# Kernel tuning notes

Measured on AMD Instinct MI355X. Metric: run time of the kernel, lower is better.

The kernel has to match this reference:

```python
import jax, jax.numpy as jnp
import numpy as np

HEADS = 16
D_MODEL = 1024
D_H = D_MODEL // HEADS


def setup_inputs() -> dict:
    key = jax.random.key(0)
    ks = jax.random.split(key, 11)
    B, S = 4, 2048
    scale = 1.0 / np.sqrt(D_MODEL)
    inp = {
        "q": jax.random.normal(ks[0], (B, S, D_MODEL), dtype=jnp.float32),
        "k": jax.random.normal(ks[1], (B, S, D_MODEL), dtype=jnp.float32),
        "v": jax.random.normal(ks[2], (B, S, D_MODEL), dtype=jnp.float32),
        "Wq": jax.random.normal(ks[3], (D_MODEL, D_MODEL), dtype=jnp.float32) * scale,
        "bq": jnp.zeros((D_MODEL,), dtype=jnp.float32),
        "Wk": jax.random.normal(ks[4], (D_MODEL, D_MODEL), dtype=jnp.float32) * scale,
        "bk": jnp.zeros((D_MODEL,), dtype=jnp.float32),
        "Wv": jax.random.normal(ks[5], (D_MODEL, D_MODEL), dtype=jnp.float32) * scale,
        "bv": jnp.zeros((D_MODEL,), dtype=jnp.float32),
        "Wo": jax.random.normal(ks[6], (D_MODEL, D_MODEL), dtype=jnp.float32) * scale,
        "bo": jnp.zeros((D_MODEL,), dtype=jnp.float32),
    }
    return inp


def reference(q, k, v, Wq, bq, Wk, bk, Wv, bv, Wo, bo):
    B, S, _ = q.shape
    # torch Linear: x @ W.T + b
    qh = (q @ Wq.T + bq).reshape(B, S, HEADS, D_H).transpose(0, 2, 1, 3)  # b h s d
    kh = (k @ Wk.T + bk).reshape(B, S, HEADS, D_H).transpose(0, 2, 1, 3)
    vh = (v @ Wv.T + bv).reshape(B, S, HEADS, D_H).transpose(0, 2, 1, 3)
    logits = jnp.einsum("bhsd,bhtd->bhst", qh, kh) / jnp.sqrt(jnp.float32(D_H))
    attn = jax.nn.softmax(logits, axis=-1)
    ctx = jnp.einsum("bhst,bhtd->bhsd", attn, vh)
    concat = ctx.transpose(0, 2, 1, 3).reshape(B, S, D_MODEL)
    return concat @ Wo.T + bo
```

## Files before the change

kernel.cpp:

```cpp
#include <hip/hip_runtime.h>
#include <hip/hip_bf16.h>
#include <stdint.h>

#define B_SZ 4
#define S_SZ 2048
#define DM   1024
#define NH   16
#define DH   64

typedef short short8 __attribute__((ext_vector_type(8)));
typedef float f32x4 __attribute__((ext_vector_type(4)));

typedef const __attribute__((address_space(1))) uint32_t* gp_t;
typedef __attribute__((address_space(3))) uint32_t* lp_t;

__device__ __forceinline__ void gload16(const void* g, void* l) {
  __builtin_amdgcn_global_load_lds((gp_t)g, (lp_t)l, 16, 0, 0);
}

__device__ __forceinline__ unsigned short f2b(float f) {
  __hip_bfloat16 h = __float2bfloat16(f);
  return *reinterpret_cast<unsigned short*>(&h);
}

__global__ void cast_acts(const float* __restrict__ a, const float* __restrict__ b,
                          const float* __restrict__ c,
                          unsigned short* __restrict__ oa, unsigned short* __restrict__ ob,
                          unsigned short* __restrict__ oc) {
  int i = blockIdx.x * blockDim.x + threadIdx.x;
  int which = i >> 21;
  int j = i & ((1 << 21) - 1);
  const float* src = which == 0 ? a : (which == 1 ? b : c);
  unsigned short* dst = which == 0 ? oa : (which == 1 ? ob : oc);
  float4 v = reinterpret_cast<const float4*>(src)[j];
  ushort4 o;
  o.x = f2b(v.x); o.y = f2b(v.y); o.z = f2b(v.z); o.w = f2b(v.w);
  reinterpret_cast<ushort4*>(dst)[j] = o;
}

__global__ void cast_w4(const float* __restrict__ a, const float* __restrict__ b,
                        const float* __restrict__ c, const float* __restrict__ d,
                        unsigned short* __restrict__ oa, unsigned short* __restrict__ ob,
                        unsigned short* __restrict__ oc, unsigned short* __restrict__ od) {
  int i = blockIdx.x * blockDim.x + threadIdx.x;
  int which = i >> 18;
  int j = i & ((1 << 18) - 1);
  const float* src = which == 0 ? a : (which == 1 ? b : (which == 2 ? c : d));
  unsigned short* dst = which == 0 ? oa : (which == 1 ? ob : (which == 2 ? oc : od));
  float4 v = reinterpret_cast<const float4*>(src)[j];
  ushort4 o;
  o.x = f2b(v.x); o.y = f2b(v.y); o.z = f2b(v.z); o.w = f2b(v.w);
  reinterpret_cast<ushort4*>(dst)[j] = o;
}

__global__ __launch_bounds__(256)
void gemm_qkv(const unsigned short* __restrict__ Aq, const unsigned short* __restrict__ Ak,
              const unsigned short* __restrict__ Av,
              const unsigned short* __restrict__ Wq, const unsigned short* __restrict__ Wk,
              const unsigned short* __restrict__ Wv,
              const float* __restrict__ bq, const float* __restrict__ bk,
              const float* __restrict__ bv,
              unsigned short* __restrict__ Qh, unsigned short* __restrict__ Kh,
              unsigned short* __restrict__ Vth, float qscale)
{
  constexpr int K = DM;
  __shared__ unsigned short lA[128 * 64];
  __shared__ unsigned short lB[128 * 64];
  const int tid  = threadIdx.x;
  const int lane = tid & 63;
  const int wave = tid >> 6;

  const int cpx = gridDim.x >> 3;
  const int bid = blockIdx.x;
  const int wg  = (bid & 7) * cpx + (bid >> 3);
  const int which = wg >> 9;
  const int rest  = wg & 511;
  const int bm = rest >> 3;
  const int bn = rest & 7;

  const unsigned short* A  = which == 0 ? Aq : (which == 1 ? Ak : Av);
  const unsigned short* Bw = which == 0 ? Wq : (which == 1 ? Wk : Wv);
  const float* bias        = which == 0 ? bq : (which == 1 ? bk : bv);
  const float scale        = which == 0 ? qscale : 1.0f;

  const int wm = (wave >> 1) << 6;
  const int wn = (wave & 1) << 6;

  f32x4 acc[4][4] = {};

  const int r0 = tid >> 3;
  const int sl = tid & 7;
  const unsigned short* Abase = A + (size_t)(bm * 128) * K;
  const unsigned short* Bbase = Bw + (size_t)(bn * 128) * K;

  for (int k0 = 0; k0 < K; k0 += 64) {
#pragma unroll
    for (int i = 0; i < 4; ++i) {
      int row = i * 32 + r0;
      int gs  = sl ^ (row & 7);
      gload16(Abase + (size_t)row * K + k0 + gs * 8, lA + (i * 256 + wave * 64) * 8);
      gload16(Bbase + (size_t)row * K + k0 + gs * 8, lB + (i * 256 + wave * 64) * 8);
    }
    __syncthreads();
#pragma unroll
    for (int ks = 0; ks < 2; ++ks) {
      short8 af[4], bf[4];
#pragma unroll
      for (int f = 0; f < 4; ++f) {
        int rowa = wm + f * 16 + (lane & 15);
        int sa   = ((ks * 4) + (lane >> 4)) ^ (rowa & 7);
        af[f] = *reinterpret_cast<const short8*>(&lA[rowa * 64 + sa * 8]);
        int rowb = wn + f * 16 + (lane & 15);
        int sb   = ((ks * 4) + (lane >> 4)) ^ (rowb & 7);
        bf[f] = *reinterpret_cast<const short8*>(&lB[rowb * 64 + sb * 8]);
      }
#pragma unroll
      for (int i = 0; i < 4; ++i)
#pragma unroll
        for (int j = 0; j < 4; ++j)
          acc[i][j] = __builtin_amdgcn_mfma_f32_16x16x32_bf16(af[i], bf[j], acc[i][j], 0, 0, 0);
    }
    __syncthreads();
  }

  float bv4[4];
#pragma unroll
  for (int j = 0; j < 4; ++j)
    bv4[j] = bias[bn * 128 + wn + j * 16 + (lane & 15)];

#pragma unroll
  for (int i = 0; i < 4; ++i) {
    int m0 = bm * 128 + wm + i * 16 + ((lane >> 4) << 2);
#pragma unroll
    for (int j = 0; j < 4; ++j) {
      int n = bn * 128 + wn + j * 16 + (lane & 15);
      if (which < 2) {
        unsigned short* o = which == 0 ? Qh : Kh;
#pragma unroll
        for (int r = 0; r < 4; ++r) {
          int m = m0 + r;
          size_t idx = ((size_t)((m >> 11) * NH + (n >> 6)) * S_SZ + (m & 2047)) * DH + (n & 63);
          o[idx] = f2b((acc[i][j][r] + bv4[j]) * scale);
        }
      } else {
        size_t idx = ((size_t)((m0 >> 11) * NH + (n >> 6)) * DH + (n & 63)) * S_SZ + (m0 & 2047);
        ushort4 pk;
        pk.x = f2b(acc[i][j][0] + bv4[j]);
        pk.y = f2b(acc[i][j][1] + bv4[j]);
        pk.z = f2b(acc[i][j][2] + bv4[j]);
        pk.w = f2b(acc[i][j][3] + bv4[j]);
        *reinterpret_cast<ushort4*>(&Vth[idx]) = pk;
      }
    }
  }
}

template<int MODE>
__global__ __launch_bounds__(256)
void gemm_bt(const unsigned short* __restrict__ A,
             const unsigned short* __restrict__ Bw,
             const float* __restrict__ bias,
             void* __restrict__ out,
             int M, int N, int K, float scale)
{
  __shared__ unsigned short lA[128 * 64];
  __shared__ unsigned short lB[128 * 64];
  const int tid  = threadIdx.x;
  const int lane = tid & 63;
  const int wave = tid >> 6;

  const int cpx = gridDim.x >> 3;
  const int bid = blockIdx.x;
  const int wg  = (bid & 7) * cpx + (bid >> 3);
  const int nbn = N >> 7;
  const int bm  = wg / nbn;
  const int bn  = wg % nbn;

  const int wm = (wave >> 1) << 6;
  const int wn = (wave & 1) << 6;

  f32x4 acc[4][4] = {};

  const int r0 = tid >> 3;
  const int sl = tid & 7;
  const unsigned short* Abase = A + (size_t)(bm * 128) * K;
  const unsigned short* Bbase = Bw + (size_t)(bn * 128) * K;

  for (int k0 = 0; k0 < K; k0 += 64) {
#pragma unroll
    for (int i = 0; i < 4; ++i) {
      int row = i * 32 + r0;
      int gs  = sl ^ (row & 7);
      gload16(Abase + (size_t)row * K + k0 + gs * 8, lA + (i * 256 + wave * 64) * 8);
      gload16(Bbase + (size_t)row * K + k0 + gs * 8, lB + (i * 256 + wave * 64) * 8);
    }
    __syncthreads();
#pragma unroll
    for (int ks = 0; ks < 2; ++ks) {
      short8 af[4], bf[4];
#pragma unroll
      for (int f = 0; f < 4; ++f) {
        int rowa = wm + f * 16 + (lane & 15);
        int sa   = ((ks * 4) + (lane >> 4)) ^ (rowa & 7);
        af[f] = *reinterpret_cast<const short8*>(&lA[rowa * 64 + sa * 8]);
        int rowb = wn + f * 16 + (lane & 15);
        int sb   = ((ks * 4) + (lane >> 4)) ^ (rowb & 7);
        bf[f] = *reinterpret_cast<const short8*>(&lB[rowb * 64 + sb * 8]);
      }
#pragma unroll
      for (int i = 0; i < 4; ++i)
#pragma unroll
        for (int j = 0; j < 4; ++j)
          acc[i][j] = __builtin_amdgcn_mfma_f32_16x16x32_bf16(af[i], bf[j], acc[i][j], 0, 0, 0);
    }
    __syncthreads();
  }

  float bv[4];
#pragma unroll
  for (int j = 0; j < 4; ++j)
    bv[j] = bias[bn * 128 + wn + j * 16 + (lane & 15)];

#pragma unroll
  for (int i = 0; i < 4; ++i) {
    int m0 = bm * 128 + wm + i * 16 + ((lane >> 4) << 2);
#pragma unroll
    for (int j = 0; j < 4; ++j) {
      int n = bn * 128 + wn + j * 16 + (lane & 15);
      float* o = (float*)out;
#pragma unroll
      for (int r = 0; r < 4; ++r)
        o[(size_t)(m0 + r) * N + n] = acc[i][j][r] + bv[j];
    }
  }
}

__global__ __launch_bounds__(256, 4)
void attn_kernel(const unsigned short* __restrict__ Q,
                 const unsigned short* __restrict__ Kc,
                 const unsigned short* __restrict__ Vt,
                 unsigned short* __restrict__ ctx)
{
  __shared__ unsigned short lK[2][64 * 64];
  __shared__ unsigned short lV[64 * 64];
  __shared__ unsigned short lP[4][16 * 64];

  const int tid  = threadIdx.x;
  const int lane = tid & 63;
  const int wave = tid >> 6;
  const int hi   = lane >> 4;
  const int lo   = lane & 15;

  const int bid = blockIdx.x;
  const int xcd = bid & 7;
  const int idx = bid >> 3;
  const int stile = idx & 15;
  const int bh    = ((idx >> 4) << 3) + xcd;
  const int b = bh >> 4, h = bh & 15;

  const int s0 = stile * 128 + wave * 32;

  short8 qf[2][2];
#pragma unroll
  for (int fm = 0; fm < 2; ++fm)
#pragma unroll
    for (int ks = 0; ks < 2; ++ks) {
      int s = s0 + fm * 16 + lo;
      int c = ks * 32 + hi * 8;
      qf[fm][ks] = *reinterpret_cast<const short8*>(&Q[((size_t)bh * S_SZ + s) * DH + c]);
    }

  f32x4 cacc[2][4] = {};
  f32x4 lacc[2] = {};

  short8 onesb;
#pragma unroll
  for (int i = 0; i < 8; ++i) onesb[i] = (short)0x3F80;

  const int r0 = tid >> 3;
  const int sl = tid & 7;
  const unsigned short* Kbh = Kc + (size_t)bh * S_SZ * DH;
  const unsigned short* Vbh = Vt + (size_t)bh * DH * S_SZ;

#define STAGE_K(bb, t0)                                                            \
  _Pragma("unroll")                                                                \
  for (int i = 0; i < 2; ++i) {                                                    \
    int row = i * 32 + r0;                                                         \
    int gs  = sl ^ (row & 7);                                                      \
    gload16(Kbh + ((size_t)(t0) + row) * DH + gs * 8, lK[bb] + (i * 256 + wave * 64) * 8); \
  }
#define STAGE_V(t0)                                                                \
  _Pragma("unroll")                                                                \
  for (int i = 0; i < 2; ++i) {                                                    \
    int row = i * 32 + r0;                                                         \
    int gs  = sl ^ (row & 7);                                                      \
    gload16(Vbh + (size_t)row * S_SZ + (t0) + gs * 8, lV + (i * 256 + wave * 64) * 8); \
  }

  STAGE_K(0, 0)

  unsigned short* Pw = &lP[wave][0];
  const int NT = S_SZ / 64;

  for (int it = 0; it < NT; ++it) {
    const int cb = it & 1;
    __syncthreads();
    STAGE_V(it * 64)
    { int nk = (it + 1 < NT) ? (it + 1) * 64 : 0;
      STAGE_K(cb ^ 1, nk) }

    f32x4 lg[4][2];
#pragma unroll
    for (int fn = 0; fn < 4; ++fn)
#pragma unroll
      for (int fm = 0; fm < 2; ++fm)
        lg[fn][fm] = f32x4{-8.f, -8.f, -8.f, -8.f};
    __builtin_amdgcn_s_setprio(1);
#pragma unroll
    for (int ks = 0; ks < 2; ++ks) {
      short8 kf[4];
#pragma unroll
      for (int fn = 0; fn < 4; ++fn) {
        int row = fn * 16 + lo;
        int s2  = ((ks * 4) + hi) ^ (row & 7);
        kf[fn] = *reinterpret_cast<const short8*>(&lK[cb][row * 64 + s2 * 8]);
      }
#pragma unroll
      for (int fn = 0; fn < 4; ++fn)
#pragma unroll
        for (int fm = 0; fm < 2; ++fm)
          lg[fn][fm] = __builtin_amdgcn_mfma_f32_16x16x32_bf16(kf[fn], qf[fm][ks], lg[fn][fm], 0, 0, 0);
    }
    __builtin_amdgcn_s_setprio(0);

    short8 pa[2][2];
    const int psw = (lo & 7) ^ (((lo >> 3) & 1) << 2);
#pragma unroll
    for (int fm = 0; fm < 2; ++fm) {
#pragma unroll
      for (int fn = 0; fn < 4; ++fn) {
        int pslot = (fn * 2 + (hi >> 1)) ^ psw;
        int paddr = lo * 64 + pslot * 8 + (hi & 1) * 4;
        ushort4 pk;
        pk.x = f2b(exp2f(lg[fn][fm][0]));
        pk.y = f2b(exp2f(lg[fn][fm][1]));
        pk.z = f2b(exp2f(lg[fn][fm][2]));
        pk.w = f2b(exp2f(lg[fn][fm][3]));
        *reinterpret_cast<ushort4*>(&Pw[paddr]) = pk;
      }
#pragma unroll
      for (int ks = 0; ks < 2; ++ks) {
        int s2 = ((ks * 4) + hi) ^ psw;
        pa[fm][ks] = *reinterpret_cast<const short8*>(&Pw[lo * 64 + s2 * 8]);
      }
    }

    asm volatile("s_waitcnt vmcnt(2)" ::: "memory");
    __builtin_amdgcn_s_barrier();
    __builtin_amdgcn_sched_barrier(0);

    __builtin_amdgcn_s_setprio(1);
#pragma unroll
    for (int ks = 0; ks < 2; ++ks) {
      short8 vbf[4];
#pragma unroll
      for (int fn = 0; fn < 4; ++fn) {
        int row = fn * 16 + lo;
        int s2  = ((ks * 4) + hi) ^ (row & 7);
        vbf[fn] = *reinterpret_cast<const short8*>(&lV[row * 64 + s2 * 8]);
      }
#pragma unroll
      for (int fm = 0; fm < 2; ++fm) {
#pragma unroll
        for (int fn = 0; fn < 4; ++fn)
          cacc[fm][fn] = __builtin_amdgcn_mfma_f32_16x16x32_bf16(pa[fm][ks], vbf[fn], cacc[fm][fn], 0, 0, 0);
        lacc[fm] = __builtin_amdgcn_mfma_f32_16x16x32_bf16(pa[fm][ks], onesb, lacc[fm], 0, 0, 0);
      }
    }
    __builtin_amdgcn_s_setprio(0);
  }

#pragma unroll
  for (int fm = 0; fm < 2; ++fm)
#pragma unroll
    for (int r = 0; r < 4; ++r) {
      float inv = 1.0f / lacc[fm][r];
      int s = s0 + fm * 16 + hi * 4 + r;
#pragma unroll
      for (int fn = 0; fn < 4; ++fn) {
        int d = fn * 16 + lo;
        ctx[(((size_t)b * S_SZ + s) * NH + h) * DH + d] = f2b(cacc[fm][fn][r] * inv);
      }
    }
}

extern "C" void kernel_launch(void* const* d_in, const int* in_sizes, int n_in,
                              void* d_out, int out_size, void* d_ws, size_t ws_size,
                              hipStream_t stream)
{
  const float* q  = (const float*)d_in[0];
  const float* k  = (const float*)d_in[1];
  const float* v  = (const float*)d_in[2];
  const float* Wq = (const float*)d_in[3];
  const float* bq = (const float*)d_in[4];
  const float* Wk = (const float*)d_in[5];
  const float* bk = (const float*)d_in[6];
  const float* Wv = (const float*)d_in[7];
  const float* bv = (const float*)d_in[8];
  const float* Wo = (const float*)d_in[9];
  const float* bo = (const float*)d_in[10];

  constexpr size_t N_ACT = (size_t)B_SZ * S_SZ * DM;
  constexpr size_t N_W   = (size_t)DM * DM;
  constexpr size_t SZ_ACT = N_ACT * 2;
  constexpr size_t SZ_W   = N_W * 2;

  char* ws = (char*)d_ws;
  unsigned short* qb  = (unsigned short*)(ws);
  unsigned short* kb  = (unsigned short*)(ws + SZ_ACT);
  unsigned short* vb_ = (unsigned short*)(ws + 2 * SZ_ACT);
  unsigned short* Wqb = (unsigned short*)(ws + 3 * SZ_ACT);
  unsigned short* Wkb = (unsigned short*)(ws + 3 * SZ_ACT + SZ_W);
  unsigned short* Wvb = (unsigned short*)(ws + 3 * SZ_ACT + 2 * SZ_W);
  unsigned short* Wob = (unsigned short*)(ws + 3 * SZ_ACT + 3 * SZ_W);
  unsigned short* Qh  = (unsigned short*)(ws + 3 * SZ_ACT + 4 * SZ_W);
  unsigned short* Kh  = (unsigned short*)(ws + 4 * SZ_ACT + 4 * SZ_W);
  unsigned short* Vth = (unsigned short*)(ws + 5 * SZ_ACT + 4 * SZ_W);
  unsigned short* ctx = qb;

  cast_acts<<<(int)(3 * (N_ACT / 4) / 256), 256, 0, stream>>>(q, k, v, qb, kb, vb_);
  cast_w4<<<(int)(4 * (N_W / 4) / 256), 256, 0, stream>>>(Wq, Wk, Wv, Wo, Wqb, Wkb, Wvb, Wob);

  const float qscale = 0.18033688011112042f;

  gemm_qkv<<<1536, 256, 0, stream>>>(qb, kb, vb_, Wqb, Wkb, Wvb, bq, bk, bv,
                                     Qh, Kh, Vth, qscale);

  attn_kernel<<<B_SZ * NH * (S_SZ / 128), 256, 0, stream>>>(Qh, Kh, Vth, ctx);

  gemm_bt<2><<<512, 256, 0, stream>>>(ctx, Wob, bo, d_out, 8192, DM, DM, 1.0f);
}
```

Baseline: 223.7 us.

## Halve attention query tile and stage K through registers into single LDS buffer

The attention kernel now processes 64 query rows per block (16 per wave) instead of 128, which doubles the grid size. K tiles are now prefetched into registers with ordinary global loads and written into one LDS buffer after the PV step, replacing the double-buffered global_load_lds path. This frees LDS and registers and adds parallelism, but it doubles K/V global traffic per query and halves the MFMA work done per staged tile.

```diff
diff --git a/kernel.cpp b/kernel.cpp
--- a/kernel.cpp
+++ b/kernel.cpp
@@ -10,6 +10,7 @@
 
 typedef short short8 __attribute__((ext_vector_type(8)));
 typedef float f32x4 __attribute__((ext_vector_type(4)));
+typedef uint32_t uint32x4 __attribute__((ext_vector_type(4)));
 
 typedef const __attribute__((address_space(1))) uint32_t* gp_t;
 typedef __attribute__((address_space(3))) uint32_t* lp_t;
@@ -241,7 +242,7 @@
                  const unsigned short* __restrict__ Vt,
                  unsigned short* __restrict__ ctx)
 {
-  __shared__ unsigned short lK[2][64 * 64];
+  __shared__ unsigned short lK[64 * 64];
   __shared__ unsigned short lV[64 * 64];
   __shared__ unsigned short lP[4][16 * 64];
 
@@ -254,24 +255,22 @@
   const int bid = blockIdx.x;
   const int xcd = bid & 7;
   const int idx = bid >> 3;
-  const int stile = idx & 15;
-  const int bh    = ((idx >> 4) << 3) + xcd;
+  const int stile = idx & 31;
+  const int bh    = ((idx >> 5) << 3) + xcd;
   const int b = bh >> 4, h = bh & 15;
 
-  const int s0 = stile * 128 + wave * 32;
-
-  short8 qf[2][2];
-#pragma unroll
-  for (int fm = 0; fm < 2; ++fm)
-#pragma unroll
-    for (int ks = 0; ks < 2; ++ks) {
-      int s = s0 + fm * 16 + lo;
-      int c = ks * 32 + hi * 8;
-      qf[fm][ks] = *reinterpret_cast<const short8*>(&Q[((size_t)bh * S_SZ + s) * DH + c]);
-    }
-
-  f32x4 cacc[2][4] = {};
-  f32x4 lacc[2] = {};
+  const int s0 = stile * 64 + wave * 16;
+
+  short8 qf[2];
+#pragma unroll
+  for (int ks = 0; ks < 2; ++ks) {
+    int s = s0 + lo;
+    int c = ks * 32 + hi * 8;
+    qf[ks] = *reinterpret_cast<const short8*>(&Q[((size_t)bh * S_SZ + s) * DH + c]);
+  }
+
+  f32x4 cacc[4] = {};
+  f32x4 lacc = {};
 
   short8 onesb;
 #pragma unroll
@@ -282,13 +281,19 @@
   const unsigned short* Kbh = Kc + (size_t)bh * S_SZ * DH;
   const unsigned short* Vbh = Vt + (size_t)bh * DH * S_SZ;
 
-#define STAGE_K(bb, t0)                                                            \
+  uint32x4 kr[2];
+
+#define LOADK(t0)                                                                  \
   _Pragma("unroll")                                                                \
   for (int i = 0; i < 2; ++i) {                                                    \
     int row = i * 32 + r0;                                                         \
     int gs  = sl ^ (row & 7);                                                      \
-    gload16(Kbh + ((size_t)(t0) + row) * DH + gs * 8, lK[bb] + (i * 256 + wave * 64) * 8); \
-  }
+    kr[i] = *reinterpret_cast<const uint32x4*>(&Kbh[((size_t)(t0) + row) * DH + gs * 8]); \
+  }
+#define WRITEK()                                                                   \
+  _Pragma("unroll")                                                                \
+  for (int i = 0; i < 2; ++i)                                                      \
+    *reinterpret_cast<uint32x4*>(&lK[i * 2048 + wave * 512 + lane * 8]) = kr[i];
 #define STAGE_V(t0)                                                                \
   _Pragma("unroll")                                                                \
   for (int i = 0; i < 2; ++i) {                                                    \
@@ -297,24 +302,24 @@
     gload16(Vbh + (size_t)row * S_SZ + (t0) + gs * 8, lV + (i * 256 + wave * 64) * 8); \
   }
 
-  STAGE_K(0, 0)
+  LOADK(0)
+  asm volatile("s_waitcnt vmcnt(0)" ::: "memory");
+  WRITEK()
 
   unsigned short* Pw = &lP[wave][0];
   const int NT = S_SZ / 64;
 
   for (int it = 0; it < NT; ++it) {
-    const int cb = it & 1;
     __syncthreads();
     STAGE_V(it * 64)
+    __builtin_amdgcn_sched_barrier(0);
     { int nk = (it + 1 < NT) ? (it + 1) * 64 : 0;
-      STAGE_K(cb ^ 1, nk) }
-
-    f32x4 lg[4][2];
+      LOADK(nk) }
+
+    f32x4 lg[4];
 #pragma unroll
     for (int fn = 0; fn < 4; ++fn)
-#pragma unroll
-      for (int fm = 0; fm < 2; ++fm)
-        lg[fn][fm] = f32x4{-8.f, -8.f, -8.f, -8.f};
+      lg[fn] = f32x4{-8.f, -8.f, -8.f, -8.f};
     __builtin_amdgcn_s_setprio(1);
 #pragma unroll
     for (int ks = 0; ks < 2; ++ks) {
@@ -323,36 +328,31 @@
       for (int fn = 0; fn < 4; ++fn) {
         int row = fn * 16 + lo;
         int s2  = ((ks * 4) + hi) ^ (row & 7);
-        kf[fn] = *reinterpret_cast<const short8*>(&lK[cb][row * 64 + s2 * 8]);
+        kf[fn] = *reinterpret_cast<const short8*>(&lK[row * 64 + s2 * 8]);
       }
 #pragma unroll
       for (int fn = 0; fn < 4; ++fn)
-#pragma unroll
-        for (int fm = 0; fm < 2; ++fm)
-          lg[fn][fm] = __builtin_amdgcn_mfma_f32_16x16x32_bf16(kf[fn], qf[fm][ks], lg[fn][fm], 0, 0, 0);
+        lg[fn] = __builtin_amdgcn_mfma_f32_16x16x32_bf16(kf[fn], qf[ks], lg[fn], 0, 0, 0);
     }
     __builtin_amdgcn_s_setprio(0);
 
-    short8 pa[2][2];
+    short8 pa[2];
     const int psw = (lo & 7) ^ (((lo >> 3) & 1) << 2);
 #pragma unroll
-    for (int fm = 0; fm < 2; ++fm) {
-#pragma unroll
-      for (int fn = 0; fn < 4; ++fn) {
-        int pslot = (fn * 2 + (hi >> 1)) ^ psw;
-        int paddr = lo * 64 + pslot * 8 + (hi & 1) * 4;
-        ushort4 pk;
-        pk.x = f2b(exp2f(lg[fn][fm][0]));
-        pk.y = f2b(exp2f(lg[fn][fm][1]));
-        pk.z = f2b(exp2f(lg[fn][fm][2]));
-        pk.w = f2b(exp2f(lg[fn][fm][3]));
-        *reinterpret_cast<ushort4*>(&Pw[paddr]) = pk;
-      }
-#pragma unroll
-      for (int ks = 0; ks < 2; ++ks) {
-        int s2 = ((ks * 4) + hi) ^ psw;
-        pa[fm][ks] = *reinterpret_cast<const short8*>(&Pw[lo * 64 + s2 * 8]);
-      }
+    for (int fn = 0; fn < 4; ++fn) {
+      int pslot = (fn * 2 + (hi >> 1)) ^ psw;
+      int paddr = lo * 64 + pslot * 8 + (hi & 1) * 4;
+      ushort4 pk;
+      pk.x = f2b(exp2f(lg[fn][0]));
+      pk.y = f2b(exp2f(lg[fn][1]));
+      pk.z = f2b(exp2f(lg[fn][2]));
+      pk.w = f2b(exp2f(lg[fn][3]));
+      *reinterpret_cast<ushort4*>(&Pw[paddr]) = pk;
+    }
+#pragma unroll
+    for (int ks = 0; ks < 2; ++ks) {
+      int s2 = ((ks * 4) + hi) ^ psw;
+      pa[ks] = *reinterpret_cast<const short8*>(&Pw[lo * 64 + s2 * 8]);
     }
 
     asm volatile("s_waitcnt vmcnt(2)" ::: "memory");
@@ -370,28 +370,26 @@
         vbf[fn] = *reinterpret_cast<const short8*>(&lV[row * 64 + s2 * 8]);
       }
 #pragma unroll
-      for (int fm = 0; fm < 2; ++fm) {
-#pragma unroll
-        for (int fn = 0; fn < 4; ++fn)
-          cacc[fm][fn] = __builtin_amdgcn_mfma_f32_16x16x32_bf16(pa[fm][ks], vbf[fn], cacc[fm][fn], 0, 0, 0);
-        lacc[fm] = __builtin_amdgcn_mfma_f32_16x16x32_bf16(pa[fm][ks], onesb, lacc[fm], 0, 0, 0);
-      }
+      for (int fn = 0; fn < 4; ++fn)
+        cacc[fn] = __builtin_amdgcn_mfma_f32_16x16x32_bf16(pa[ks], vbf[fn], cacc[fn], 0, 0, 0);
+      lacc = __builtin_amdgcn_mfma_f32_16x16x32_bf16(pa[ks], onesb, lacc, 0, 0, 0);
     }
     __builtin_amdgcn_s_setprio(0);
-  }
-
-#pragma unroll
-  for (int fm = 0; fm < 2; ++fm)
-#pragma unroll
-    for (int r = 0; r < 4; ++r) {
-      float inv = 1.0f / lacc[fm][r];
-      int s = s0 + fm * 16 + hi * 4 + r;
-#pragma unroll
-      for (int fn = 0; fn < 4; ++fn) {
-        int d = fn * 16 + lo;
-        ctx[(((size_t)b * S_SZ + s) * NH + h) * DH + d] = f2b(cacc[fm][fn][r] * inv);
-      }
-    }
+
+    asm volatile("s_waitcnt vmcnt(0)" ::: "memory");
+    WRITEK()
+  }
+
+#pragma unroll
+  for (int r = 0; r < 4; ++r) {
+    float inv = 1.0f / lacc[r];
+    int s = s0 + hi * 4 + r;
+#pragma unroll
+    for (int fn = 0; fn < 4; ++fn) {
+      int d = fn * 16 + lo;
+      ctx[(((size_t)b * S_SZ + s) * NH + h) * DH + d] = f2b(cacc[fn][r] * inv);
+    }
+  }
 }
 
 extern "C" void kernel_launch(void* const* d_in, const int* in_sizes, int n_in,
@@ -436,7 +434,7 @@
   gemm_qkv<<<1536, 256, 0, stream>>>(qb, kb, vb_, Wqb, Wkb, Wvb, bq, bk, bv,
                                      Qh, Kh, Vth, qscale);
 
-  attn_kernel<<<B_SZ * NH * (S_SZ / 128), 256, 0, stream>>>(Qh, Kh, Vth, ctx);
+  attn_kernel<<<B_SZ * NH * (S_SZ / 64), 256, 0, stream>>>(Qh, Kh, Vth, ctx);
 
   gemm_bt<2><<<512, 256, 0, stream>>>(ctx, Wob, bo, d_out, 8192, DM, DM, 1.0f);
 }
```

Measured after the change: 230.6 us. 3.1% more time.

## Double KV tile to 128 and prefetch K through registers

Applied to the files above, without the earlier changes.

The attention loop now handles 128 keys per iteration instead of 64, halving the number of iterations and barriers. K tiles are prefetched into registers with plain global loads and written to a single LDS buffer after the PV stage, replacing the double-buffered global-to-LDS loads. V staging uses a wider 128-column layout with a new swizzle. This raises register pressure and LDS footprint, which may reduce occupancy under the launch bounds of 4 blocks per CU.

```diff
diff --git a/kernel.cpp b/kernel.cpp
--- a/kernel.cpp
+++ b/kernel.cpp
@@ -10,6 +10,7 @@
 
 typedef short short8 __attribute__((ext_vector_type(8)));
 typedef float f32x4 __attribute__((ext_vector_type(4)));
+typedef uint32_t uint32x4 __attribute__((ext_vector_type(4)));
 
 typedef const __attribute__((address_space(1))) uint32_t* gp_t;
 typedef __attribute__((address_space(3))) uint32_t* lp_t;
@@ -241,8 +242,8 @@
                  const unsigned short* __restrict__ Vt,
                  unsigned short* __restrict__ ctx)
 {
-  __shared__ unsigned short lK[2][64 * 64];
-  __shared__ unsigned short lV[64 * 64];
+  __shared__ unsigned short lK[128 * 64];
+  __shared__ unsigned short lV[64 * 128];
   __shared__ unsigned short lP[4][16 * 64];
 
   const int tid  = threadIdx.x;
@@ -282,92 +283,103 @@
   const unsigned short* Kbh = Kc + (size_t)bh * S_SZ * DH;
   const unsigned short* Vbh = Vt + (size_t)bh * DH * S_SZ;
 
-#define STAGE_K(bb, t0)                                                            \
+  uint32x4 kr[4];
+
+#define LOADK(t0)                                                                  \
   _Pragma("unroll")                                                                \
-  for (int i = 0; i < 2; ++i) {                                                    \
+  for (int i = 0; i < 4; ++i) {                                                    \
     int row = i * 32 + r0;                                                         \
     int gs  = sl ^ (row & 7);                                                      \
-    gload16(Kbh + ((size_t)(t0) + row) * DH + gs * 8, lK[bb] + (i * 256 + wave * 64) * 8); \
-  }
+    kr[i] = *reinterpret_cast<const uint32x4*>(&Kbh[((size_t)(t0) + row) * DH + gs * 8]); \
+  }
+#define WRITEK()                                                                   \
+  _Pragma("unroll")                                                                \
+  for (int i = 0; i < 4; ++i)                                                      \
+    *reinterpret_cast<uint32x4*>(&lK[i * 2048 + wave * 512 + lane * 8]) = kr[i];
 #define STAGE_V(t0)                                                                \
   _Pragma("unroll")                                                                \
-  for (int i = 0; i < 2; ++i) {                                                    \
-    int row = i * 32 + r0;                                                         \
-    int gs  = sl ^ (row & 7);                                                      \
-    gload16(Vbh + (size_t)row * S_SZ + (t0) + gs * 8, lV + (i * 256 + wave * 64) * 8); \
-  }
-
-  STAGE_K(0, 0)
+  for (int i = 0; i < 4; ++i) {                                                    \
+    int rowv = i * 16 + wave * 4 + hi;                                             \
+    int gsv  = lo ^ (wave * 4 + hi);                                               \
+    gload16(Vbh + (size_t)rowv * S_SZ + (t0) + gsv * 8, lV + (i * 256 + wave * 64) * 8); \
+  }
+
+  LOADK(0)
+  asm volatile("s_waitcnt vmcnt(0)" ::: "memory");
+  WRITEK()
 
   unsigned short* Pw = &lP[wave][0];
-  const int NT = S_SZ / 64;
+  const int NT = S_SZ / 128;
 
   for (int it = 0; it < NT; ++it) {
-    const int cb = it & 1;
     __syncthreads();
-    STAGE_V(it * 64)
-    { int nk = (it + 1 < NT) ? (it + 1) * 64 : 0;
-      STAGE_K(cb ^ 1, nk) }
-
-    f32x4 lg[4][2];
-#pragma unroll
-    for (int fn = 0; fn < 4; ++fn)
-#pragma unroll
-      for (int fm = 0; fm < 2; ++fm)
-        lg[fn][fm] = f32x4{-8.f, -8.f, -8.f, -8.f};
-    __builtin_amdgcn_s_setprio(1);
-#pragma unroll
-    for (int ks = 0; ks < 2; ++ks) {
-      short8 kf[4];
-#pragma unroll
-      for (int fn = 0; fn < 4; ++fn) {
-        int row = fn * 16 + lo;
-        int s2  = ((ks * 4) + hi) ^ (row & 7);
-        kf[fn] = *reinterpret_cast<const short8*>(&lK[cb][row * 64 + s2 * 8]);
-      }
-#pragma unroll
-      for (int fn = 0; fn < 4; ++fn)
+    STAGE_V(it * 128)
+    __builtin_amdgcn_sched_barrier(0);
+    { int nk = (it + 1 < NT) ? (it + 1) * 128 : 0;
+      LOADK(nk) }
+
+    short8 pa[2][4];
+    const int psw = (lo & 7) ^ (((lo >> 3) & 1) << 2);
+#pragma unroll
+    for (int hh = 0; hh < 2; ++hh) {
+      f32x4 lg[4][2];
+#pragma unroll
+      for (int f = 0; f < 4; ++f)
 #pragma unroll
         for (int fm = 0; fm < 2; ++fm)
-          lg[fn][fm] = __builtin_amdgcn_mfma_f32_16x16x32_bf16(kf[fn], qf[fm][ks], lg[fn][fm], 0, 0, 0);
-    }
-    __builtin_amdgcn_s_setprio(0);
-
-    short8 pa[2][2];
-    const int psw = (lo & 7) ^ (((lo >> 3) & 1) << 2);
-#pragma unroll
-    for (int fm = 0; fm < 2; ++fm) {
-#pragma unroll
-      for (int fn = 0; fn < 4; ++fn) {
-        int pslot = (fn * 2 + (hi >> 1)) ^ psw;
-        int paddr = lo * 64 + pslot * 8 + (hi & 1) * 4;
-        ushort4 pk;
-        pk.x = f2b(exp2f(lg[fn][fm][0]));
-        pk.y = f2b(exp2f(lg[fn][fm][1]));
-        pk.z = f2b(exp2f(lg[fn][fm][2]));
-        pk.w = f2b(exp2f(lg[fn][fm][3]));
-        *reinterpret_cast<ushort4*>(&Pw[paddr]) = pk;
-      }
+          lg[f][fm] = f32x4{-8.f, -8.f, -8.f, -8.f};
+      __builtin_amdgcn_s_setprio(1);
 #pragma unroll
       for (int ks = 0; ks < 2; ++ks) {
-        int s2 = ((ks * 4) + hi) ^ psw;
-        pa[fm][ks] = *reinterpret_cast<const short8*>(&Pw[lo * 64 + s2 * 8]);
-      }
-    }
-
-    asm volatile("s_waitcnt vmcnt(2)" ::: "memory");
+        short8 kf[4];
+#pragma unroll
+        for (int f = 0; f < 4; ++f) {
+          int rowk = (hh * 4 + f) * 16 + lo;
+          int s2   = ((ks * 4) + hi) ^ (rowk & 7);
+          kf[f] = *reinterpret_cast<const short8*>(&lK[rowk * 64 + s2 * 8]);
+        }
+#pragma unroll
+        for (int f = 0; f < 4; ++f)
+#pragma unroll
+          for (int fm = 0; fm < 2; ++fm)
+            lg[f][fm] = __builtin_amdgcn_mfma_f32_16x16x32_bf16(kf[f], qf[fm][ks], lg[f][fm], 0, 0, 0);
+      }
+      __builtin_amdgcn_s_setprio(0);
+
+#pragma unroll
+      for (int fm = 0; fm < 2; ++fm) {
+#pragma unroll
+        for (int f = 0; f < 4; ++f) {
+          int pslot = (f * 2 + (hi >> 1)) ^ psw;
+          int paddr = lo * 64 + pslot * 8 + (hi & 1) * 4;
+          ushort4 pk;
+          pk.x = f2b(exp2f(lg[f][fm][0]));
+          pk.y = f2b(exp2f(lg[f][fm][1]));
+          pk.z = f2b(exp2f(lg[f][fm][2]));
+          pk.w = f2b(exp2f(lg[f][fm][3]));
+          *reinterpret_cast<ushort4*>(&Pw[paddr]) = pk;
+        }
+#pragma unroll
+        for (int kh = 0; kh < 2; ++kh) {
+          int s2 = ((kh * 4) + hi) ^ psw;
+          pa[fm][hh * 2 + kh] = *reinterpret_cast<const short8*>(&Pw[lo * 64 + s2 * 8]);
+        }
+      }
+    }
+
+    asm volatile("s_waitcnt vmcnt(4)" ::: "memory");
     __builtin_amdgcn_s_barrier();
     __builtin_amdgcn_sched_barrier(0);
 
     __builtin_amdgcn_s_setprio(1);
 #pragma unroll
-    for (int ks = 0; ks < 2; ++ks) {
+    for (int ks = 0; ks < 4; ++ks) {
       short8 vbf[4];
 #pragma unroll
       for (int fn = 0; fn < 4; ++fn) {
-        int row = fn * 16 + lo;
-        int s2  = ((ks * 4) + hi) ^ (row & 7);
-        vbf[fn] = *reinterpret_cast<const short8*>(&lV[row * 64 + s2 * 8]);
+        int rowv = fn * 16 + lo;
+        int s2   = ((ks * 4) + hi) ^ lo;
+        vbf[fn] = *reinterpret_cast<const short8*>(&lV[rowv * 128 + s2 * 8]);
       }
 #pragma unroll
       for (int fm = 0; fm < 2; ++fm) {
@@ -378,6 +390,9 @@
       }
     }
     __builtin_amdgcn_s_setprio(0);
+
+    asm volatile("s_waitcnt vmcnt(0)" ::: "memory");
+    WRITEK()
   }
 
 #pragma unroll
```

Measured after the change: 388.6 us. 1.74x slower.

## Split attention over key halves and merge partial contexts in a separate kernel

Applied to the files above, without the earlier changes.

Each attention block now handles only half of the key sequence, which doubles the grid and writes unnormalized bf16 context plus row sums per half. A new merge kernel adds the two partial contexts and divides by the summed denominators. K staging changes from async global-to-LDS double buffering to a register prefetch written to a single LDS buffer after the PV step, which frees LDS. This buys more parallelism and occupancy at the cost of an extra kernel pass over the context and extra bf16 rounding of the partial sums. The merge is valid without max tracking because the softmax logits use a fixed offset.

```diff
diff --git a/kernel.cpp b/kernel.cpp
--- a/kernel.cpp
+++ b/kernel.cpp
@@ -10,6 +10,7 @@
 
 typedef short short8 __attribute__((ext_vector_type(8)));
 typedef float f32x4 __attribute__((ext_vector_type(4)));
+typedef uint32_t uint32x4 __attribute__((ext_vector_type(4)));
 
 typedef const __attribute__((address_space(1))) uint32_t* gp_t;
 typedef __attribute__((address_space(3))) uint32_t* lp_t;
@@ -21,6 +22,10 @@
 __device__ __forceinline__ unsigned short f2b(float f) {
   __hip_bfloat16 h = __float2bfloat16(f);
   return *reinterpret_cast<unsigned short*>(&h);
+}
+__device__ __forceinline__ float b2f(unsigned short u) {
+  uint32_t w = (uint32_t)u << 16;
+  return __builtin_bit_cast(float, w);
 }
 
 __global__ void cast_acts(const float* __restrict__ a, const float* __restrict__ b,
@@ -239,9 +244,12 @@
 void attn_kernel(const unsigned short* __restrict__ Q,
                  const unsigned short* __restrict__ Kc,
                  const unsigned short* __restrict__ Vt,
-                 unsigned short* __restrict__ ctx)
+                 unsigned short* __restrict__ c0,
+                 unsigned short* __restrict__ c1,
+                 float* __restrict__ l0,
+                 float* __restrict__ l1)
 {
-  __shared__ unsigned short lK[2][64 * 64];
+  __shared__ unsigned short lK[64 * 64];
   __shared__ unsigned short lV[64 * 64];
   __shared__ unsigned short lP[4][16 * 64];
 
@@ -254,11 +262,13 @@
   const int bid = blockIdx.x;
   const int xcd = bid & 7;
   const int idx = bid >> 3;
-  const int stile = idx & 15;
-  const int bh    = ((idx >> 4) << 3) + xcd;
+  const int half  = idx & 1;
+  const int stile = (idx >> 1) & 15;
+  const int bh    = ((idx >> 5) << 3) + xcd;
   const int b = bh >> 4, h = bh & 15;
 
   const int s0 = stile * 128 + wave * 32;
+  const int tbase = half * (S_SZ / 2);
 
   short8 qf[2][2];
 #pragma unroll
@@ -282,13 +292,19 @@
   const unsigned short* Kbh = Kc + (size_t)bh * S_SZ * DH;
   const unsigned short* Vbh = Vt + (size_t)bh * DH * S_SZ;
 
-#define STAGE_K(bb, t0)                                                            \
+  uint32x4 kr[2];
+
+#define LOADK(t0)                                                                  \
   _Pragma("unroll")                                                                \
   for (int i = 0; i < 2; ++i) {                                                    \
     int row = i * 32 + r0;                                                         \
     int gs  = sl ^ (row & 7);                                                      \
-    gload16(Kbh + ((size_t)(t0) + row) * DH + gs * 8, lK[bb] + (i * 256 + wave * 64) * 8); \
-  }
+    kr[i] = *reinterpret_cast<const uint32x4*>(&Kbh[((size_t)(t0) + row) * DH + gs * 8]); \
+  }
+#define WRITEK()                                                                   \
+  _Pragma("unroll")                                                                \
+  for (int i = 0; i < 2; ++i)                                                      \
+    *reinterpret_cast<uint32x4*>(&lK[i * 2048 + wave * 512 + lane * 8]) = kr[i];
 #define STAGE_V(t0)                                                                \
   _Pragma("unroll")                                                                \
   for (int i = 0; i < 2; ++i) {                                                    \
@@ -297,17 +313,19 @@
     gload16(Vbh + (size_t)row * S_SZ + (t0) + gs * 8, lV + (i * 256 + wave * 64) * 8); \
   }
 
-  STAGE_K(0, 0)
+  LOADK(tbase)
+  asm volatile("s_waitcnt vmcnt(0)" ::: "memory");
+  WRITEK()
 
   unsigned short* Pw = &lP[wave][0];
-  const int NT = S_SZ / 64;
+  const int NT = (S_SZ / 2) / 64;
 
   for (int it = 0; it < NT; ++it) {
-    const int cb = it & 1;
     __syncthreads();
-    STAGE_V(it * 64)
-    { int nk = (it + 1 < NT) ? (it + 1) * 64 : 0;
-      STAGE_K(cb ^ 1, nk) }
+    STAGE_V(tbase + it * 64)
+    __builtin_amdgcn_sched_barrier(0);
+    { int nk = (it + 1 < NT) ? tbase + (it + 1) * 64 : tbase;
+      LOADK(nk) }
 
     f32x4 lg[4][2];
 #pragma unroll
@@ -323,7 +341,7 @@
       for (int fn = 0; fn < 4; ++fn) {
         int row = fn * 16 + lo;
         int s2  = ((ks * 4) + hi) ^ (row & 7);
-        kf[fn] = *reinterpret_cast<const short8*>(&lK[cb][row * 64 + s2 * 8]);
+        kf[fn] = *reinterpret_cast<const short8*>(&lK[row * 64 + s2 * 8]);
       }
 #pragma unroll
       for (int fn = 0; fn < 4; ++fn)
@@ -378,20 +396,51 @@
       }
     }
     __builtin_amdgcn_s_setprio(0);
-  }
-
+
+    asm volatile("s_waitcnt vmcnt(0)" ::: "memory");
+    WRITEK()
+  }
+
+  unsigned short* cdst = half ? c1 : c0;
+  float* ldst = half ? l1 : l0;
 #pragma unroll
   for (int fm = 0; fm < 2; ++fm)
 #pragma unroll
     for (int r = 0; r < 4; ++r) {
-      float inv = 1.0f / lacc[fm][r];
       int s = s0 + fm * 16 + hi * 4 + r;
 #pragma unroll
       for (int fn = 0; fn < 4; ++fn) {
         int d = fn * 16 + lo;
-        ctx[(((size_t)b * S_SZ + s) * NH + h) * DH + d] = f2b(cacc[fm][fn][r] * inv);
-      }
-    }
+        cdst[(((size_t)b * S_SZ + s) * NH + h) * DH + d] = f2b(cacc[fm][fn][r]);
+      }
+      if (lo == 0) ldst[(size_t)bh * S_SZ + s] = lacc[fm][r];
+    }
+}
+
+__global__ void merge_ctx(const unsigned short* __restrict__ c0,
+                          const unsigned short* __restrict__ c1,
+                          const float* __restrict__ l0,
+                          const float* __restrict__ l1,
+                          unsigned short* __restrict__ ctx)
+{
+  int i = blockIdx.x * blockDim.x + threadIdx.x;
+  int rh = i >> 3;
+  int h  = rh & 15;
+  int bs = rh >> 4;
+  int s  = bs & 2047;
+  int b  = bs >> 11;
+  float l = l0[(size_t)(b * 16 + h) * S_SZ + s] + l1[(size_t)(b * 16 + h) * S_SZ + s];
+  float inv = 1.0f / l;
+  short8 a0 = *reinterpret_cast<const short8*>(&c0[(size_t)i * 8]);
+  short8 a1 = *reinterpret_cast<const short8*>(&c1[(size_t)i * 8]);
+  ushort4 o[2];
+#pragma unroll
+  for (int j = 0; j < 8; ++j) {
+    float v = (b2f((unsigned short)a0[j]) + b2f((unsigned short)a1[j])) * inv;
+    ((unsigned short*)o)[j] = f2b(v);
+  }
+  *reinterpret_cast<short8*>(&ctx[(size_t)i * 8]) =
+      *reinterpret_cast<const short8*>(&o[0]);
 }
 
 extern "C" void kernel_launch(void* const* d_in, const int* in_sizes, int n_in,
@@ -426,7 +475,12 @@
   unsigned short* Qh  = (unsigned short*)(ws + 3 * SZ_ACT + 4 * SZ_W);
   unsigned short* Kh  = (unsigned short*)(ws + 4 * SZ_ACT + 4 * SZ_W);
   unsigned short* Vth = (unsigned short*)(ws + 5 * SZ_ACT + 4 * SZ_W);
+
   unsigned short* ctx = qb;
+  unsigned short* c0  = kb;
+  unsigned short* c1  = vb_;
+  float* l0 = (float*)Wqb;
+  float* l1 = (float*)Wkb;
 
   cast_acts<<<(int)(3 * (N_ACT / 4) / 256), 256, 0, stream>>>(q, k, v, qb, kb, vb_);
   cast_w4<<<(int)(4 * (N_W / 4) / 256), 256, 0, stream>>>(Wq, Wk, Wv, Wo, Wqb, Wkb, Wvb, Wob);
@@ -436,7 +490,10 @@
   gemm_qkv<<<1536, 256, 0, stream>>>(qb, kb, vb_, Wqb, Wkb, Wvb, bq, bk, bv,
                                      Qh, Kh, Vth, qscale);
 
-  attn_kernel<<<B_SZ * NH * (S_SZ / 128), 256, 0, stream>>>(Qh, Kh, Vth, ctx);
+  attn_kernel<<<B_SZ * NH * (S_SZ / 128) * 2, 256, 0, stream>>>(Qh, Kh, Vth,
+                                                                c0, c1, l0, l1);
+
+  merge_ctx<<<(int)(N_ACT / 8 / 256), 256, 0, stream>>>(c0, c1, l0, l1, ctx);
 
   gemm_bt<2><<<512, 256, 0, stream>>>(ctx, Wob, bo, d_out, 8192, DM, DM, 1.0f);
 }
```

Measured after the change: 247.8 us. 10.8% more time.
